# Optimization experiments

Measured on AMD Instinct MI355X. Metric: run time of the kernel, lower is better.

## Reference

```python
import jax, jax.numpy as jnp
import numpy as np

B, S, D, H = 4, 2048, 1024, 16
HD = D // H


def setup_inputs() -> dict:
    key = jax.random.key(0)
    ks = jax.random.split(key, 12)
    sc = 0.02
    inp = {
        "q": jax.random.normal(ks[0], (B, S, D), jnp.float32),
        "k": jax.random.normal(ks[1], (B, S, D), jnp.float32),
        "v": jax.random.normal(ks[2], (B, S, D), jnp.float32),
        "mask": jnp.tril(jnp.ones((S, S), jnp.int32))[None, None],  # causal [1,1,S,S]
        "Wq": jax.random.normal(ks[3], (D, D), jnp.float32) * sc,
        "bq": jnp.zeros((D,), jnp.float32),
        "Wk": jax.random.normal(ks[4], (D, D), jnp.float32) * sc,
        "bk": jnp.zeros((D,), jnp.float32),
        "Wv": jax.random.normal(ks[5], (D, D), jnp.float32) * sc,
        "bv": jnp.zeros((D,), jnp.float32),
        "Wo": jax.random.normal(ks[6], (D, D), jnp.float32) * sc,
        "bo": jnp.zeros((D,), jnp.float32),
    }
    return inp


def reference(q, k, v, mask, Wq, bq, Wk, bk, Wv, bv, Wo, bo):
    # Linear projections (torch Linear: x @ W.T + b)
    qh = (q @ Wq.T + bq).reshape(B, S, H, HD).transpose(0, 2, 1, 3)  # [B,H,S,hd]
    kh = (k @ Wk.T + bk).reshape(B, S, H, HD).transpose(0, 2, 1, 3)
    vh = (v @ Wv.T + bv).reshape(B, S, H, HD).transpose(0, 2, 1, 3)
    score = jnp.einsum("bhqd,bhkd->bhqk", qh, kh) / jnp.sqrt(jnp.float32(HD))
    score = jnp.where(mask == 0, jnp.float32(-10000.0), score)
    attn = jax.nn.softmax(score, axis=-1)
    out = jnp.einsum("bhqk,bhkd->bhqd", attn, vh)  # [B,H,S,hd]
    out = out.transpose(0, 2, 1, 3).reshape(B, S, D)
    return out @ Wo.T + bo
```

## Files before the change

kernel.cpp:

```cpp
#include <hip/hip_runtime.h>

#define S_LEN 2048
#define D_DIM 1024
#define NB    4
#define NH    16
#define HDIM  64
#define QSCL  0.18033688011112042f

typedef float  f32x4  __attribute__((ext_vector_type(4)));
typedef __bf16 bf16x4 __attribute__((ext_vector_type(4)));
typedef __bf16 bf16x8 __attribute__((ext_vector_type(8)));

static __device__ __forceinline__ f32x4 mfma16(bf16x8 a, bf16x8 b, f32x4 c) {
  return __builtin_amdgcn_mfma_f32_16x16x32_bf16(a, b, c, 0, 0, 0);
}
static __device__ __forceinline__ bf16x4 cvt4(f32x4 v) {
  return __builtin_convertvector(v, bf16x4);
}
static __device__ __forceinline__ bf16x8 cvt8(f32x4 lo, f32x4 hi) {
  bf16x4 a = cvt4(lo), b = cvt4(hi);
  bf16x8 r;
  r[0] = a[0]; r[1] = a[1]; r[2] = a[2]; r[3] = a[3];
  r[4] = b[0]; r[5] = b[1]; r[6] = b[2]; r[7] = b[3];
  return r;
}
static __device__ __forceinline__ void cp16(const void* g, void* l) {
  __builtin_amdgcn_global_load_lds(
      (const __attribute__((address_space(1))) unsigned int*)g,
      (__attribute__((address_space(3))) unsigned int*)l, 16, 0, 0);
}

__global__ __launch_bounds__(256) void conv_w(
    const float* __restrict__ Wq, const float* __restrict__ Wk,
    const float* __restrict__ Wv, const float* __restrict__ Wo,
    __bf16* __restrict__ out)
{
  const float* src;
  if (blockIdx.y == 0) src = Wq;
  else if (blockIdx.y == 1) src = Wk;
  else if (blockIdx.y == 2) src = Wv;
  else src = Wo;
  size_t i = ((size_t)blockIdx.x * 256 + threadIdx.x) * 4;
  f32x4 v = *(const f32x4*)(src + i);
  *(bf16x4*)(out + (size_t)blockIdx.y * (D_DIM * D_DIM) + i) = cvt4(v);
}

__global__ __launch_bounds__(256) void conv_a(
    const float* __restrict__ q, const float* __restrict__ k,
    const float* __restrict__ v, __bf16* __restrict__ out)
{
  const float* src;
  if (blockIdx.y == 0) src = q;
  else if (blockIdx.y == 1) src = k;
  else src = v;
  size_t i = ((size_t)blockIdx.x * 256 + threadIdx.x) * 4;
  f32x4 x = *(const f32x4*)(src + i);
  *(bf16x4*)(out + (size_t)blockIdx.y * ((size_t)NB * S_LEN * D_DIM) + i) = cvt4(x);
}

static __device__ __forceinline__ void proj_epilogue(
    f32x4 (&acc)[4][4], int z, int mbase, int nbase, int wm, int wn,
    int l15, int quad, const float* bias,
    __bf16* qh, __bf16* kh, __bf16* vt)
{
  const float scl = (z == 0) ? QSCL : 1.0f;
#pragma unroll
  for (int mt = 0; mt < 4; ++mt)
#pragma unroll
    for (int nt = 0; nt < 4; ++nt) {
      int n = nbase + wn + nt * 16 + l15;
      int h = n >> 6, hd = n & 63;
      float bb = bias[n];
      f32x4 vv = acc[mt][nt];
#pragma unroll
      for (int r = 0; r < 4; ++r) vv[r] = (vv[r] + bb) * scl;
      bf16x4 pv = cvt4(vv);
      int m0 = mbase + wm + mt * 16 + quad * 4;
      int b = m0 >> 11, s0 = m0 & 2047;
      if (z == 2) {
        *(bf16x4*)(vt + ((size_t)((b * NH + h) * HDIM + hd)) * S_LEN + s0) = pv;
      } else {
        __bf16* out = (z == 0) ? qh : kh;
#pragma unroll
        for (int r = 0; r < 4; ++r)
          out[((size_t)(b * NH + h) * S_LEN + s0 + r) * HDIM + hd] = pv[r];
      }
    }
}

__global__ __launch_bounds__(256, 4) void proj_bf16(
    const __bf16* __restrict__ abf, const __bf16* __restrict__ Wbf,
    const float* __restrict__ bq, const float* __restrict__ bk, const float* __restrict__ bv,
    __bf16* __restrict__ qh, __bf16* __restrict__ kh, __bf16* __restrict__ vt)
{
  const __bf16* A = abf + (size_t)blockIdx.z * ((size_t)NB * S_LEN * D_DIM);
  const __bf16* W = Wbf + (size_t)blockIdx.z * (D_DIM * D_DIM);
  const float* bias = (blockIdx.z == 0) ? bq : (blockIdx.z == 1) ? bk : bv;

  __shared__ __bf16 As[128 * 64];
  __shared__ __bf16 Bs[128 * 64];

  const int tid  = threadIdx.x;
  const int wave = tid >> 6;
  const int lane = tid & 63;
  const int l15  = lane & 15;
  const int quad = lane >> 4;
  const int mbase = blockIdx.x * 128;
  const int nbase = blockIdx.y * 128;
  const int wm = (wave & 1) * 64;
  const int wn = (wave >> 1) * 64;
  const int brow = lane >> 3;
  const int scol = ((lane & 7) ^ (brow & 7)) * 8;
  const int swz  = l15 & 7;

  f32x4 acc[4][4] = {};

  for (int kt = 0; kt < D_DIM; kt += 64) {
#pragma unroll
    for (int c = 0; c < 4; ++c) {
      int r = wave * 32 + c * 8 + brow;
      cp16(A + (size_t)(mbase + r) * D_DIM + kt + scol, As + r * 64);
      cp16(W + (size_t)(nbase + r) * D_DIM + kt + scol, Bs + r * 64);
    }
    __syncthreads();

#pragma unroll
    for (int k0 = 0; k0 < 2; ++k0) {
      bf16x8 af[4], bfr[4];
#pragma unroll
      for (int i = 0; i < 4; ++i) {
        int off = ((k0 * 4 + quad) ^ swz) * 8;
        af[i]  = *(const bf16x8*)(As + (wm + i * 16 + l15) * 64 + off);
        bfr[i] = *(const bf16x8*)(Bs + (wn + i * 16 + l15) * 64 + off);
      }
#pragma unroll
      for (int mt = 0; mt < 4; ++mt)
#pragma unroll
        for (int nt = 0; nt < 4; ++nt)
          acc[mt][nt] = mfma16(af[mt], bfr[nt], acc[mt][nt]);
    }
    __syncthreads();
  }

  proj_epilogue(acc, blockIdx.z, mbase, nbase, wm, wn, l15, quad, bias, qh, kh, vt);
}

__global__ __launch_bounds__(256, 2) void proj_f32(
    const float* __restrict__ qin, const float* __restrict__ kin, const float* __restrict__ vin,
    const __bf16* __restrict__ Wbf,
    const float* __restrict__ bq, const float* __restrict__ bk, const float* __restrict__ bv,
    __bf16* __restrict__ qh, __bf16* __restrict__ kh, __bf16* __restrict__ vt)
{
  const float* A; const float* bias;
  if (blockIdx.z == 0)      { A = qin; bias = bq; }
  else if (blockIdx.z == 1) { A = kin; bias = bk; }
  else                      { A = vin; bias = bv; }
  const __bf16* W = Wbf + (size_t)blockIdx.z * (D_DIM * D_DIM);

  __shared__ float  As[128 * 64];
  __shared__ __bf16 Bs[128 * 64];

  const int tid  = threadIdx.x;
  const int wave = tid >> 6;
  const int lane = tid & 63;
  const int l15  = lane & 15;
  const int quad = lane >> 4;
  const int mbase = blockIdx.x * 128;
  const int nbase = blockIdx.y * 128;
  const int wm = (wave & 1) * 64;
  const int wn = (wave >> 1) * 64;
  const int arow = lane >> 4;
  const int brow = lane >> 3;

  f32x4 acc[4][4] = {};

  for (int kt = 0; kt < D_DIM; kt += 64) {
#pragma unroll
    for (int c = 0; c < 8; ++c) {
      int rr = c * 4 + arow;
      int r  = wave * 32 + rr;
      int col = ((lane & 15) ^ (rr & 15)) * 4;
      cp16(A + (size_t)(mbase + r) * D_DIM + kt + col, As + r * 64);
    }
#pragma unroll
    for (int c = 0; c < 4; ++c) {
      int r  = wave * 32 + c * 8 + brow;
      int col = ((lane & 7) ^ (brow & 7)) * 8;
      cp16(W + (size_t)(nbase + r) * D_DIM + kt + col, Bs + r * 64);
    }
    __syncthreads();

#pragma unroll
    for (int k0 = 0; k0 < 2; ++k0) {
      bf16x8 af[4], bfr[4];
#pragma unroll
      for (int i = 0; i < 4; ++i) {
        const float* ap = As + (wm + i * 16 + l15) * 64;
        int c0 = k0 * 8 + quad * 2;
        f32x4 lo = *(const f32x4*)(ap + ((c0 ^ l15) * 4));
        f32x4 hi = *(const f32x4*)(ap + (((c0 + 1) ^ l15) * 4));
        af[i] = cvt8(lo, hi);
        bfr[i] = *(const bf16x8*)(Bs + (wn + i * 16 + l15) * 64 +
                                  (((k0 * 4 + quad) ^ (l15 & 7)) * 8));
      }
#pragma unroll
      for (int mt = 0; mt < 4; ++mt)
#pragma unroll
        for (int nt = 0; nt < 4; ++nt)
          acc[mt][nt] = mfma16(af[mt], bfr[nt], acc[mt][nt]);
    }
    __syncthreads();
  }

  proj_epilogue(acc, blockIdx.z, mbase, nbase, wm, wn, l15, quad, bias, qh, kh, vt);
}

__global__ __launch_bounds__(256, 4) void attn_kernel(
    const __bf16* __restrict__ qh, const __bf16* __restrict__ kh,
    const __bf16* __restrict__ vt, __bf16* __restrict__ ao)
{
  __shared__ __bf16 Kb[2][64 * 64];
  __shared__ __bf16 Vb[2][64 * 64];

  const int lin = blockIdx.x + (blockIdx.y << 4);
  const int xcd = lin & 7;
  const int idx = lin >> 3;
  const int u   = idx & 15;
  const int x   = (u & 1) ? (15 - (u >> 1)) : (u >> 1);
  const int bh  = xcd * 8 + (idx >> 4);

  const int qc0 = x, qc1 = 31 - x;
  const int last = qc1;

  const __bf16* qp = qh + (size_t)bh * S_LEN * HDIM;
  const __bf16* kp = kh + (size_t)bh * S_LEN * HDIM;
  const __bf16* vp = vt + (size_t)bh * HDIM * S_LEN;

  const int tid  = threadIdx.x;
  const int wave = tid >> 6;
  const int lane = tid & 63;
  const int l15  = lane & 15;
  const int quad = lane >> 4;
  const int w16  = wave * 16;
  const int srow = lane >> 3;
  const int swz  = l15 & 7;
  const int vswz = ((l15 >> 3) << 2) | (l15 & 3);
  const int kr0  = ((l15 >> 2) << 3) | (l15 & 3);
  const int b = bh >> 4, h = bh & 15;

  bf16x8 fq[2][2];
#pragma unroll
  for (int j = 0; j < 2; ++j) {
    const int qb = (j ? qc1 : qc0) * 64;
    const __bf16* qrow = qp + (size_t)(qb + w16 + l15) * HDIM;
    fq[j][0] = *(const bf16x8*)(qrow + quad * 8);
    fq[j][1] = *(const bf16x8*)(qrow + 32 + quad * 8);
  }

  f32x4 accO[2][4] = {};
  float lp[2] = {0.f, 0.f};

#pragma unroll
  for (int c = 0; c < 2; ++c) {
    int rb = w16 + c * 8;
    int sc2 = (((lane & 7) ^ (((c & 1) << 2) | (srow & 3)))) * 8;
    cp16(kp + (size_t)(rb + srow) * HDIM + sc2, &Kb[0][rb * 64]);
    cp16(vp + (size_t)(rb + srow) * S_LEN + sc2, &Vb[0][rb * 64]);
  }

  int cur = 0;
  for (int kt = 0; kt <= last; ++kt) {
    __syncthreads();

    if (kt < last) {
#pragma unroll
      for (int c = 0; c < 2; ++c) {
        int rb = w16 + c * 8;
        int sc2 = (((lane & 7) ^ (((c & 1) << 2) | (srow & 3)))) * 8;
        cp16(kp + (size_t)((kt + 1) * 64 + rb + srow) * HDIM + sc2,
             &Kb[cur ^ 1][rb * 64]);
        cp16(vp + (size_t)(rb + srow) * S_LEN + (kt + 1) * 64 + sc2,
             &Vb[cur ^ 1][rb * 64]);
      }
    }

    const __bf16* Kc = &Kb[cur][0];
    const __bf16* Vc = &Vb[cur][0];
    const bool act0 = (kt <= qc0);

    f32x4 sc[2][4] = {};
#pragma unroll
    for (int k0 = 0; k0 < 2; ++k0)
#pragma unroll
      for (int nt = 0; nt < 4; ++nt) {
        const int krow = kr0 + ((nt & 1) << 2) + ((nt >> 1) << 5);
        bf16x8 bk = *(const bf16x8*)(Kc + krow * 64 +
                                     (((k0 * 4 + quad) ^ swz) * 8));
        if (act0) sc[0][nt] = mfma16(bk, fq[0][k0], sc[0][nt]);
        sc[1][nt] = mfma16(bk, fq[1][k0], sc[1][nt]);
      }

    bf16x8 pa[2][2];
#pragma unroll
    for (int j = 0; j < 2; ++j) {
      if (j == 0 && !act0) continue;
      const int qcj = j ? qc1 : qc0;
      f32x4 pf[4];
#pragma unroll
      for (int nt = 0; nt < 4; ++nt) {
#pragma unroll
        for (int r = 0; r < 4; ++r) pf[nt][r] = __builtin_amdgcn_exp2f(sc[j][nt][r]);
        if (kt == qcj) {
#pragma unroll
          for (int r = 0; r < 4; ++r) {
            int key = ((nt >> 1) << 5) + (quad << 3) + ((nt & 1) << 2) + r;
            if (key > w16 + l15) pf[nt][r] = 0.f;
          }
        }
      }
      f32x4 lv = (pf[0] + pf[1]) + (pf[2] + pf[3]);
      lp[j] += (lv[0] + lv[1]) + (lv[2] + lv[3]);
      pa[j][0] = cvt8(pf[0], pf[1]);
      pa[j][1] = cvt8(pf[2], pf[3]);
    }

#pragma unroll
    for (int k0 = 0; k0 < 2; ++k0)
#pragma unroll
      for (int nt = 0; nt < 4; ++nt) {
        bf16x8 bv = *(const bf16x8*)(Vc + (nt * 16 + l15) * 64 +
                                     (((k0 * 4 + quad) ^ vswz) * 8));
        if (act0) accO[0][nt] = mfma16(pa[0][k0], bv, accO[0][nt]);
        accO[1][nt] = mfma16(pa[1][k0], bv, accO[1][nt]);
      }

    cur ^= 1;
  }

#pragma unroll
  for (int j = 0; j < 2; ++j) {
    float lf = lp[j];
    lf += __shfl_xor(lf, 16);
    lf += __shfl_xor(lf, 32);
    const int qb = (j ? qc1 : qc0) * 64;
#pragma unroll
    for (int r = 0; r < 4; ++r) {
      float inv = 1.0f / __shfl(lf, quad * 4 + r);
#pragma unroll
      for (int nt = 0; nt < 4; ++nt) accO[j][nt][r] *= inv;
    }
#pragma unroll
    for (int nt = 0; nt < 4; ++nt) {
      bf16x4 ob = cvt4(accO[j][nt]);
#pragma unroll
      for (int r = 0; r < 4; ++r) {
        int sr = qb + w16 + quad * 4 + r;
        ao[((size_t)b * S_LEN + sr) * D_DIM + h * HDIM + nt * 16 + l15] = ob[r];
      }
    }
  }
}

__global__ __launch_bounds__(256, 4) void out_gemm(
    const __bf16* __restrict__ Ain, const __bf16* __restrict__ Wbf,
    const float* __restrict__ bo, float* __restrict__ Cout)
{
  __shared__ __bf16 As[128 * 64];
  __shared__ __bf16 Bs[128 * 64];

  const int tid  = threadIdx.x;
  const int wave = tid >> 6;
  const int lane = tid & 63;
  const int l15  = lane & 15;
  const int quad = lane >> 4;
  const int mbase = blockIdx.x * 128;
  const int nbase = blockIdx.y * 128;
  const int wm = (wave & 1) * 64;
  const int wn = (wave >> 1) * 64;
  const int brow = lane >> 3;
  const int scol = ((lane & 7) ^ (brow & 7)) * 8;
  const int swz  = l15 & 7;

  f32x4 acc[4][4] = {};

  for (int kt = 0; kt < D_DIM; kt += 64) {
#pragma unroll
    for (int c = 0; c < 4; ++c) {
      int r = wave * 32 + c * 8 + brow;
      cp16(Ain + (size_t)(mbase + r) * D_DIM + kt + scol, As + r * 64);
      cp16(Wbf + (size_t)(nbase + r) * D_DIM + kt + scol, Bs + r * 64);
    }
    __syncthreads();

#pragma unroll
    for (int k0 = 0; k0 < 2; ++k0) {
      bf16x8 af[4], bfr[4];
#pragma unroll
      for (int i = 0; i < 4; ++i) {
        int off = ((k0 * 4 + quad) ^ swz) * 8;
        af[i]  = *(const bf16x8*)(As + (wm + i * 16 + l15) * 64 + off);
        bfr[i] = *(const bf16x8*)(Bs + (wn + i * 16 + l15) * 64 + off);
      }
#pragma unroll
      for (int mt = 0; mt < 4; ++mt)
#pragma unroll
        for (int nt = 0; nt < 4; ++nt)
          acc[mt][nt] = mfma16(af[mt], bfr[nt], acc[mt][nt]);
    }
    __syncthreads();
  }

#pragma unroll
  for (int mt = 0; mt < 4; ++mt)
#pragma unroll
    for (int nt = 0; nt < 4; ++nt) {
      int n = nbase + wn + nt * 16 + l15;
      float bb = bo[n];
      int m0 = mbase + wm + mt * 16 + quad * 4;
#pragma unroll
      for (int r = 0; r < 4; ++r)
        Cout[(size_t)(m0 + r) * D_DIM + n] = acc[mt][nt][r] + bb;
    }
}

extern "C" void kernel_launch(void* const* d_in, const int* in_sizes, int n_in,
                              void* d_out, int out_size, void* d_ws, size_t ws_size,
                              hipStream_t stream) {
  const float* q  = (const float*)d_in[0];
  const float* k  = (const float*)d_in[1];
  const float* v  = (const float*)d_in[2];
  const float* Wq = (const float*)d_in[4];
  const float* bq = (const float*)d_in[5];
  const float* Wk = (const float*)d_in[6];
  const float* bk = (const float*)d_in[7];
  const float* Wv = (const float*)d_in[8];
  const float* bv = (const float*)d_in[9];
  const float* Wo = (const float*)d_in[10];
  const float* bo = (const float*)d_in[11];

  __bf16* ws = (__bf16*)d_ws;
  const size_t WSZ = (size_t)D_DIM * D_DIM;
  const size_t NE  = (size_t)NB * S_LEN * D_DIM;
  __bf16* wbf = ws;
  __bf16* qh  = ws + 4 * WSZ;
  __bf16* kh  = qh + NE;
  __bf16* vt  = kh + NE;
  __bf16* ao  = vt + NE;
  __bf16* abf = vt + NE;
  const size_t NEED = (size_t)(4 * WSZ + 6 * NE) * sizeof(__bf16);

  const bool useBf16A = (ws_size >= NEED);

  conv_w<<<dim3(1024, 4), 256, 0, stream>>>(Wq, Wk, Wv, Wo, wbf);
  if (useBf16A) {
    conv_a<<<dim3(8192, 3), 256, 0, stream>>>(q, k, v, abf);
    proj_bf16<<<dim3(64, 8, 3), 256, 0, stream>>>(abf, wbf, bq, bk, bv, qh, kh, vt);
  } else {
    proj_f32<<<dim3(64, 8, 3), 256, 0, stream>>>(q, k, v, wbf, bq, bk, bv, qh, kh, vt);
  }
  attn_kernel<<<dim3(16, 64), 256, 0, stream>>>(qh, kh, vt, ao);
  out_gemm<<<dim3(64, 8), 256, 0, stream>>>(ao, wbf + 3 * WSZ, bo, (float*)d_out);
}
```

Before: 306.1 us.

## Drop separate activation bf16 conversion, always use fused f32 projection; add MFMA priority hints

Removes the conv_a pre-pass and the bf16-input projection GEMM, so the projection always reads fp32 activations and converts them in-kernel. This avoids writing and re-reading a bf16 copy of q/k/v, trading it for heavier fp32 loads inside the GEMM. proj_f32 launch bounds are raised from 2 to 3 blocks per CU, and s_setprio hints are placed around the MFMA sections of the attention loop to favour matrix-core issue across waves.

Measured after the change: 303.7 us. No clear change (-0.8%).

```diff
diff --git a/kernel.cpp b/kernel.cpp
--- a/kernel.cpp
+++ b/kernel.cpp
@@ -45,19 +45,6 @@
   *(bf16x4*)(out + (size_t)blockIdx.y * (D_DIM * D_DIM) + i) = cvt4(v);
 }
 
-__global__ __launch_bounds__(256) void conv_a(
-    const float* __restrict__ q, const float* __restrict__ k,
-    const float* __restrict__ v, __bf16* __restrict__ out)
-{
-  const float* src;
-  if (blockIdx.y == 0) src = q;
-  else if (blockIdx.y == 1) src = k;
-  else src = v;
-  size_t i = ((size_t)blockIdx.x * 256 + threadIdx.x) * 4;
-  f32x4 x = *(const f32x4*)(src + i);
-  *(bf16x4*)(out + (size_t)blockIdx.y * ((size_t)NB * S_LEN * D_DIM) + i) = cvt4(x);
-}
-
 static __device__ __forceinline__ void proj_epilogue(
     f32x4 (&acc)[4][4], int z, int mbase, int nbase, int wm, int wn,
     int l15, int quad, const float* bias,
@@ -88,64 +75,7 @@
     }
 }
 
-__global__ __launch_bounds__(256, 4) void proj_bf16(
-    const __bf16* __restrict__ abf, const __bf16* __restrict__ Wbf,
-    const float* __restrict__ bq, const float* __restrict__ bk, const float* __restrict__ bv,
-    __bf16* __restrict__ qh, __bf16* __restrict__ kh, __bf16* __restrict__ vt)
-{
-  const __bf16* A = abf + (size_t)blockIdx.z * ((size_t)NB * S_LEN * D_DIM);
-  const __bf16* W = Wbf + (size_t)blockIdx.z * (D_DIM * D_DIM);
-  const float* bias = (blockIdx.z == 0) ? bq : (blockIdx.z == 1) ? bk : bv;
-
-  __shared__ __bf16 As[128 * 64];
-  __shared__ __bf16 Bs[128 * 64];
-
-  const int tid  = threadIdx.x;
-  const int wave = tid >> 6;
-  const int lane = tid & 63;
-  const int l15  = lane & 15;
-  const int quad = lane >> 4;
-  const int mbase = blockIdx.x * 128;
-  const int nbase = blockIdx.y * 128;
-  const int wm = (wave & 1) * 64;
-  const int wn = (wave >> 1) * 64;
-  const int brow = lane >> 3;
-  const int scol = ((lane & 7) ^ (brow & 7)) * 8;
-  const int swz  = l15 & 7;
-
-  f32x4 acc[4][4] = {};
-
-  for (int kt = 0; kt < D_DIM; kt += 64) {
-#pragma unroll
-    for (int c = 0; c < 4; ++c) {
-      int r = wave * 32 + c * 8 + brow;
-      cp16(A + (size_t)(mbase + r) * D_DIM + kt + scol, As + r * 64);
-      cp16(W + (size_t)(nbase + r) * D_DIM + kt + scol, Bs + r * 64);
-    }
-    __syncthreads();
-
-#pragma unroll
-    for (int k0 = 0; k0 < 2; ++k0) {
-      bf16x8 af[4], bfr[4];
-#pragma unroll
-      for (int i = 0; i < 4; ++i) {
-        int off = ((k0 * 4 + quad) ^ swz) * 8;
-        af[i]  = *(const bf16x8*)(As + (wm + i * 16 + l15) * 64 + off);
-        bfr[i] = *(const bf16x8*)(Bs + (wn + i * 16 + l15) * 64 + off);
-      }
-#pragma unroll
-      for (int mt = 0; mt < 4; ++mt)
-#pragma unroll
-        for (int nt = 0; nt < 4; ++nt)
-          acc[mt][nt] = mfma16(af[mt], bfr[nt], acc[mt][nt]);
-    }
-    __syncthreads();
-  }
-
-  proj_epilogue(acc, blockIdx.z, mbase, nbase, wm, wn, l15, quad, bias, qh, kh, vt);
-}
-
-__global__ __launch_bounds__(256, 2) void proj_f32(
+__global__ __launch_bounds__(256, 3) void proj_f32(
     const float* __restrict__ qin, const float* __restrict__ kin, const float* __restrict__ vin,
     const __bf16* __restrict__ Wbf,
     const float* __restrict__ bq, const float* __restrict__ bk, const float* __restrict__ bv,
@@ -289,6 +219,7 @@
     const bool act0 = (kt <= qc0);
 
     f32x4 sc[2][4] = {};
+    __builtin_amdgcn_s_setprio(1);
 #pragma unroll
     for (int k0 = 0; k0 < 2; ++k0)
 #pragma unroll
@@ -299,6 +230,7 @@
         if (act0) sc[0][nt] = mfma16(bk, fq[0][k0], sc[0][nt]);
         sc[1][nt] = mfma16(bk, fq[1][k0], sc[1][nt]);
       }
+    __builtin_amdgcn_s_setprio(0);
 
     bf16x8 pa[2][2];
 #pragma unroll
@@ -324,6 +256,7 @@
       pa[j][1] = cvt8(pf[2], pf[3]);
     }
 
+    __builtin_amdgcn_s_setprio(1);
 #pragma unroll
     for (int k0 = 0; k0 < 2; ++k0)
 #pragma unroll
@@ -333,6 +266,7 @@
         if (act0) accO[0][nt] = mfma16(pa[0][k0], bv, accO[0][nt]);
         accO[1][nt] = mfma16(pa[1][k0], bv, accO[1][nt]);
       }
+    __builtin_amdgcn_s_setprio(0);
 
     cur ^= 1;
   }
@@ -446,18 +380,9 @@
   __bf16* kh  = qh + NE;
   __bf16* vt  = kh + NE;
   __bf16* ao  = vt + NE;
-  __bf16* abf = vt + NE;
-  const size_t NEED = (size_t)(4 * WSZ + 6 * NE) * sizeof(__bf16);
-
-  const bool useBf16A = (ws_size >= NEED);
 
   conv_w<<<dim3(1024, 4), 256, 0, stream>>>(Wq, Wk, Wv, Wo, wbf);
-  if (useBf16A) {
-    conv_a<<<dim3(8192, 3), 256, 0, stream>>>(q, k, v, abf);
-    proj_bf16<<<dim3(64, 8, 3), 256, 0, stream>>>(abf, wbf, bq, bk, bv, qh, kh, vt);
-  } else {
-    proj_f32<<<dim3(64, 8, 3), 256, 0, stream>>>(q, k, v, wbf, bq, bk, bv, qh, kh, vt);
-  }
+  proj_f32<<<dim3(64, 8, 3), 256, 0, stream>>>(q, k, v, wbf, bq, bk, bv, qh, kh, vt);
   attn_kernel<<<dim3(16, 64), 256, 0, stream>>>(qh, kh, vt, ao);
   out_gemm<<<dim3(64, 8), 256, 0, stream>>>(ao, wbf + 3 * WSZ, bo, (float*)d_out);
 }
```
